# Kernel optimization log

Hardware: AMD Instinct MI355X
Metric: run time of the kernel (lower is better)

## Reference

```python
import math
import jax, jax.numpy as jnp
import numpy as np

# Dimensions (scalar irreps: o3.Irreps('8x0e').dim == 8, FullyConnectedTensorProduct
# between scalar irreps reduces to a learned bilinear map with a 3D weight tensor)
N = 50000       # nodes
C = 4           # channel dim ('c' in the einsum 'nci,neio->nceo')
DI = 8          # irreps_in.dim
DE = 8          # irreps_edge_attr.dim (must equal DI for the einsum to typecheck)
DO = 8          # irreps_out.dim (must equal DI for lin2 to consume the messages)
DA = 16         # irreps_node_attr.dim
E = 400000      # edges
F_EDGE = 32     # number_of_edge_features
H = 64          # radial_neurons
NUM_NEIGHBORS = 8


def setup_inputs() -> dict:
    key = jax.random.key(0)
    ks = jax.random.split(key, 12)
    inv = lambda f: 1.0 / np.sqrt(f)
    return {
        "node_input": jax.random.normal(ks[0], (N, C, DI), jnp.float32),
        "node_attr": jax.random.normal(ks[1], (N, DA), jnp.float32),
        "edge_features": jax.random.normal(ks[2], (E, F_EDGE), jnp.float32),
        # bilinear tensor-product weights (sc, lin1, lin2)
        "W_sc": jax.random.normal(ks[3], (DI, DA, DO), jnp.float32) * inv(DI * DA),
        "W_lin1": jax.random.normal(ks[4], (DI, DA, DI), jnp.float32) * inv(DI * DA),
        "W_lin2": jax.random.normal(ks[5], (DO, DA, DO), jnp.float32) * inv(DO * DA),
        # radial MLP: Linear(F_EDGE,H) -> SiLU -> Linear(H, DI*DE*DO)
        "fc_w1": jax.random.normal(ks[6], (F_EDGE, H), jnp.float32) * inv(F_EDGE),
        "fc_b1": jnp.zeros((H,), jnp.float32),
        "fc_w2": jax.random.normal(ks[7], (H, DI * DE * DO), jnp.float32) * inv(H),
        "fc_b2": jnp.zeros((DI * DE * DO,), jnp.float32),
        "edge_src": jax.random.randint(ks[8], (E,), 0, N, jnp.int32),
        "edge_dst": jax.random.randint(ks[9], (E,), 0, N, jnp.int32),
    }


def reference(node_input, node_attr, edge_features, W_sc, W_lin1, W_lin2,
              fc_w1, fc_b1, fc_w2, fc_b2, edge_src, edge_dst):
    n_nodes = node_input.shape[0]
    # self-connection and input linear (bilinear in node feature & node attr)
    s = jnp.einsum('nci,na,iao->nco', node_input, node_attr, W_sc)      # [N,C,DO]
    x = jnp.einsum('nci,na,iaj->ncj', node_input, node_attr, W_lin1)    # [N,C,DI]
    # radial MLP -> per-edge weight tensor [E, DI, DE, DO]
    h = jax.nn.silu(edge_features @ fc_w1 + fc_b1)
    ef = (h @ fc_w2 + fc_b2).reshape(-1, DI, DE, DO)
    # gather by source, per-edge contraction (einsum 'nci,neio->nceo'):
    # contract x's irrep dim with ef axis 2, keep ef axis 1 as output dim d
    msg = jnp.einsum('eci,edio->ecdo', x[edge_src], ef)                 # [E,C,DI,DO]
    # scatter-add to destination nodes
    agg = jax.ops.segment_sum(msg, edge_dst, num_segments=n_nodes)      # [N,C,DI,DO]
    agg = agg / jnp.sqrt(jnp.asarray(NUM_NEIGHBORS, agg.dtype))
    # output linear on the last (irreps_out) axis
    x2 = jnp.einsum('ncdo,na,oap->ncdp', agg, node_attr, W_lin2)        # [N,C,DI,DO]
    c_s = math.sin(math.pi / 8.0)
    # fully-connected scalar-irrep TP -> output_mask is all ones -> c_x scalar
    c_x = math.cos(math.pi / 8.0)
    return c_s * s[:, :, None, :] + c_x * x2
```

## Files before the change

kernel.cpp:

```cpp
#include <hip/hip_runtime.h>
#include <math.h>

#define CC 4
#define FE 32
#define HH 64
#define EBS 256
#define KEXT 544
#define ASTR 69

typedef __attribute__((ext_vector_type(8))) short bf16x8;
typedef __attribute__((ext_vector_type(4))) float f32x4;

__device__ inline unsigned short f2bf(float f) {
    unsigned u = __float_as_uint(f);
    u += 0x7fffu + ((u >> 16) & 1u);
    return (unsigned short)(u >> 16);
}
__device__ inline float bf2f(unsigned short b) {
    return __uint_as_float(((unsigned)b) << 16);
}

__global__ __launch_bounds__(256) void k_nodeprep(
    const float* __restrict__ node_input, const float* __restrict__ node_attr,
    const float* __restrict__ W_lin1, const float* __restrict__ W_sc,
    const float* __restrict__ W_lin2,
    float* __restrict__ xbuf, float* __restrict__ sbuf,
    float* __restrict__ w2n_ws, int N)
{
    const float c_s = 0.3826834323650898f;
    const float c_x_scaled = 0.9238795325112867f * 0.35355339059327373f;
    int node = blockIdx.x * 4 + (threadIdx.x >> 6);
    int lane = threadIdx.x & 63;
    if (node >= N) return;

    float attr_own = (lane < 16) ? node_attr[(size_t)node * 16 + lane] : 0.f;
    float ni_own   = (lane < 32) ? node_input[(size_t)node * 32 + lane] : 0.f;

    int iw = lane >> 3, jw = lane & 7;
    float wb1 = 0.f, wbs = 0.f, w2n = 0.f;
    #pragma unroll
    for (int a = 0; a < 16; ++a) {
        float fa = __shfl(attr_own, a);
        int idx = (iw * 16 + a) * 8 + jw;
        wb1 += fa * W_lin1[idx];
        wbs += fa * W_sc[idx];
        w2n += fa * W_lin2[idx];
    }
    w2n_ws[(size_t)node * 64 + lane] = c_x_scaled * w2n;

    int c_ = (lane >> 3) & 3, jo = lane & 7;
    float xo = 0.f, so = 0.f;
    #pragma unroll
    for (int i = 0; i < 8; ++i) {
        float niv = __shfl(ni_own, c_ * 8 + i);
        xo += niv * __shfl(wb1, i * 8 + jo);
        so += niv * __shfl(wbs, i * 8 + jo);
    }
    if (lane < 32) {
        xbuf[(size_t)node * 32 + lane] = xo;
        sbuf[(size_t)node * 32 + lane] = c_s * so;
    }
}

__global__ __launch_bounds__(256) void k_hist(
    const int* __restrict__ edge_dst, int* __restrict__ counts, int E)
{
    int e = blockIdx.x * 256 + threadIdx.x;
    if (e < E) atomicAdd(&counts[edge_dst[e]], 1);
}

__global__ __launch_bounds__(1024) void k_scanA(
    const int* __restrict__ counts, int* __restrict__ offsets,
    int* __restrict__ btot, int N)
{
    __shared__ int wsum[16];
    __shared__ int wpre[16];
    int tid = threadIdx.x, wid = tid >> 6, lane = tid & 63;
    int idx = blockIdx.x * 1024 + tid;
    int v = (idx < N) ? counts[idx] : 0;
    int x = v;
    #pragma unroll
    for (int s = 1; s < 64; s <<= 1) {
        int y = __shfl_up(x, s);
        if (lane >= s) x += y;
    }
    if (lane == 63) wsum[wid] = x;
    __syncthreads();
    if (wid == 0) {
        int wv = (lane < 16) ? wsum[lane] : 0;
        int wx = wv;
        #pragma unroll
        for (int s = 1; s < 16; s <<= 1) {
            int y = __shfl_up(wx, s);
            if (lane >= s) wx += y;
        }
        if (lane < 16) wpre[lane] = wx - wv;
    }
    __syncthreads();
    int excl = wpre[wid] + (x - v);
    if (idx < N) offsets[idx] = excl;
    if (tid == 1023) btot[blockIdx.x] = excl + v;
}

__global__ __launch_bounds__(1024) void k_scanB(int* __restrict__ btot, int nb)
{
    __shared__ int wsum[16];
    __shared__ int wpre[16];
    int tid = threadIdx.x, wid = tid >> 6, lane = tid & 63;
    int v = (tid < nb) ? btot[tid] : 0;
    int x = v;
    #pragma unroll
    for (int s = 1; s < 64; s <<= 1) {
        int y = __shfl_up(x, s);
        if (lane >= s) x += y;
    }
    if (lane == 63) wsum[wid] = x;
    __syncthreads();
    if (wid == 0) {
        int wv = (lane < 16) ? wsum[lane] : 0;
        int wx = wv;
        #pragma unroll
        for (int s = 1; s < 16; s <<= 1) {
            int y = __shfl_up(wx, s);
            if (lane >= s) wx += y;
        }
        if (lane < 16) wpre[lane] = wx - wv;
    }
    __syncthreads();
    if (tid < nb) btot[tid] = wpre[wid] + (x - v);
}

__global__ __launch_bounds__(256) void k_scanC(
    int* __restrict__ offsets, const int* __restrict__ btot,
    int* __restrict__ cursor, int N)
{
    int i = blockIdx.x * 256 + threadIdx.x;
    if (i < N) {
        int o = offsets[i] + btot[i >> 10];
        offsets[i] = o;
        cursor[i] = o;
    }
}

__global__ __launch_bounds__(256) void k_fill(
    const int* __restrict__ edge_dst, const int* __restrict__ edge_src,
    int* __restrict__ cursor, int* __restrict__ srcs, int* __restrict__ epos, int E)
{
    int e = blockIdx.x * 256 + threadIdx.x;
    if (e < E) {
        int pos = atomicAdd(&cursor[edge_dst[e]], 1);
        srcs[pos] = edge_src[e];
        epos[e] = pos;
    }
}

__global__ __launch_bounds__(256) void k_xgather(
    const int* __restrict__ srcs, const float* __restrict__ xin,
    float* __restrict__ xg, int E)
{
    int t = blockIdx.x * 256 + threadIdx.x;
    if (t >= E * 4) return;
    int pos = t >> 2, q = t & 3;
    int src = srcs[pos];
    const float4* xp = reinterpret_cast<const float4*>(xin + (size_t)src * 32 + q * 8);
    float4 a = xp[0], b = xp[1];
    float4* op = reinterpret_cast<float4*>(xg + (size_t)pos * 32 + q * 8);
    op[0] = a; op[1] = b;
}

__global__ __launch_bounds__(256) void k_prep_bfrag(
    const float* __restrict__ fc_w2, const float* __restrict__ fc_b2,
    unsigned short* __restrict__ Bfrag)
{
    int t = blockIdx.x * 256 + threadIdx.x;
    if (t >= KEXT * 64) return;
    int kappa = t >> 6, nu = t & 63;
    int d = nu >> 3, o = nu & 7;
    float val;
    if (kappa < 512)      val = fc_w2[(size_t)(kappa >> 3) * 512 + d * 64 + (kappa & 7) * 8 + o];
    else if (kappa < 520) val = fc_b2[d * 64 + (kappa & 7) * 8 + o];
    else                  val = 0.f;
    int kk = kappa >> 5;
    int lane = ((kappa >> 3) & 3) * 16 + (nu & 15);
    int ct = nu >> 4;
    int j = kappa & 7;
    Bfrag[(size_t)((kk * 4 + ct) * 64 + lane) * 8 + j] = f2bf(val);
}

__global__ __launch_bounds__(256) void k_prep_bfrag1(
    const float* __restrict__ fc_w1, unsigned short* __restrict__ Bfrag1)
{
    int t = blockIdx.x * 256 + threadIdx.x;
    if (t >= 4 * 64 * 8) return;
    int j = t & 7, l = (t >> 3) & 63, ct = t >> 9;
    int k = (l >> 4) * 8 + j;
    int n = ct * 16 + (l & 15);
    Bfrag1[t] = f2bf(fc_w1[(size_t)k * HH + n]);
}

__global__ __launch_bounds__(256) void k_hsilu(
    const float* __restrict__ edge_features,
    const unsigned short* __restrict__ Bfrag1, const float* __restrict__ fc_b1,
    const int* __restrict__ epos,
    unsigned short* __restrict__ H, int E)
{
    int wid = threadIdx.x >> 6, lane = threadIdx.x & 63;
    int e0 = (blockIdx.x * 4 + wid) * 16;
    if (e0 >= E) return;

    bf16x8 b[4];
    #pragma unroll
    for (int ct = 0; ct < 4; ++ct) {
        uint4 bv = reinterpret_cast<const uint4*>(Bfrag1)[ct * 64 + lane];
        b[ct] = *reinterpret_cast<bf16x8*>(&bv);
    }
    float bias[4];
    #pragma unroll
    for (int ct = 0; ct < 4; ++ct) bias[ct] = fc_b1[ct * 16 + (lane & 15)];

    int pr[4];
    #pragma unroll
    for (int v = 0; v < 4; ++v) {
        int r = e0 + (lane >> 4) * 4 + v;
        pr[v] = (r < E) ? epos[r] : -1;
    }

    int row = e0 + (lane & 15);
    if (row >= E) row = E - 1;
    const float4* ap = reinterpret_cast<const float4*>(
        edge_features + (size_t)row * FE + (lane >> 4) * 8);
    float4 a0 = ap[0], a1 = ap[1];
    unsigned au[4];
    au[0] = (unsigned)f2bf(a0.x) | ((unsigned)f2bf(a0.y) << 16);
    au[1] = (unsigned)f2bf(a0.z) | ((unsigned)f2bf(a0.w) << 16);
    au[2] = (unsigned)f2bf(a1.x) | ((unsigned)f2bf(a1.y) << 16);
    au[3] = (unsigned)f2bf(a1.z) | ((unsigned)f2bf(a1.w) << 16);
    bf16x8 a = *reinterpret_cast<bf16x8*>(au);

    f32x4 acc[4];
    #pragma unroll
    for (int ct = 0; ct < 4; ++ct) {
        acc[ct] = (f32x4){0.f, 0.f, 0.f, 0.f};
        acc[ct] = __builtin_amdgcn_mfma_f32_16x16x32_bf16(a, b[ct], acc[ct], 0, 0, 0);
    }

    #pragma unroll
    for (int ct = 0; ct < 4; ++ct) {
        #pragma unroll
        for (int v = 0; v < 4; ++v) {
            if (pr[v] >= 0) {
                float x = acc[ct][v] + bias[ct];
                float s = x / (1.f + __expf(-x));
                H[(size_t)pr[v] * HH + ct * 16 + (lane & 15)] = f2bf(s);
            }
        }
    }
}

__global__ __launch_bounds__(256) void k_zgemm(
    const unsigned short* __restrict__ H, const float* __restrict__ xg,
    const int* __restrict__ offsets, const int* __restrict__ counts,
    const unsigned short* __restrict__ Bfrag,
    float* __restrict__ out, int N)
{
    __shared__ uint4 alds[16 * ASTR];
    int wid = threadIdx.x >> 6, lane = threadIdx.x & 63;
    int node = blockIdx.x * 4 + wid;
    bool valid = (node < N);

    float z[CC][8];
    #pragma unroll
    for (int c = 0; c < CC; ++c)
        #pragma unroll
        for (int i = 0; i < 8; ++i) z[c][i] = 0.f;
    float xsown = 0.f;

    int off = 0, cnt = 0;
    if (valid) { off = offsets[node]; cnt = counts[node]; }
    #pragma unroll 2
    for (int j = 0; j < cnt; ++j) {
        size_t pos = (size_t)(off + j);
        float hk = bf2f(H[pos * HH + lane]);
        const float4* xp = reinterpret_cast<const float4*>(xg + pos * 32);
        float xs[32];
        #pragma unroll
        for (int q = 0; q < 8; ++q) {
            float4 v = xp[q];
            xs[q * 4 + 0] = v.x; xs[q * 4 + 1] = v.y;
            xs[q * 4 + 2] = v.z; xs[q * 4 + 3] = v.w;
        }
        #pragma unroll
        for (int c = 0; c < CC; ++c)
            #pragma unroll
            for (int i = 0; i < 8; ++i)
                z[c][i] += hk * xs[c * 8 + i];
        xsown += xg[pos * 32 + (lane & 31)];
    }

    #pragma unroll
    for (int c = 0; c < CC; ++c) {
        uint4 pk;
        pk.x = (unsigned)f2bf(z[c][0]) | ((unsigned)f2bf(z[c][1]) << 16);
        pk.y = (unsigned)f2bf(z[c][2]) | ((unsigned)f2bf(z[c][3]) << 16);
        pk.z = (unsigned)f2bf(z[c][4]) | ((unsigned)f2bf(z[c][5]) << 16);
        pk.w = (unsigned)f2bf(z[c][6]) | ((unsigned)f2bf(z[c][7]) << 16);
        alds[(wid * 4 + c) * ASTR + lane] = pk;
    }
    float xb[8];
    #pragma unroll
    for (int i = 0; i < 8; ++i) xb[i] = __shfl(xsown, (lane & 3) * 8 + i);
    int r4 = wid * 4;
    if (lane < 4) {
        uint4 pk;
        pk.x = (unsigned)f2bf(xb[0]) | ((unsigned)f2bf(xb[1]) << 16);
        pk.y = (unsigned)f2bf(xb[2]) | ((unsigned)f2bf(xb[3]) << 16);
        pk.z = (unsigned)f2bf(xb[4]) | ((unsigned)f2bf(xb[5]) << 16);
        pk.w = (unsigned)f2bf(xb[6]) | ((unsigned)f2bf(xb[7]) << 16);
        alds[(r4 + lane) * ASTR + 64] = pk;
    } else if (lane < 16) {
        int j = lane - 4;
        uint4 zz; zz.x = 0u; zz.y = 0u; zz.z = 0u; zz.w = 0u;
        alds[(r4 + (j & 3)) * ASTR + 65 + (j >> 2)] = zz;
    }

    bf16x8 bfr[17];
    #pragma unroll
    for (int kk = 0; kk < 16; ++kk) {
        uint4 bv = reinterpret_cast<const uint4*>(Bfrag)[(kk * 4 + wid) * 64 + lane];
        bfr[kk] = *reinterpret_cast<bf16x8*>(&bv);
    }
    {
        uint4 bv = reinterpret_cast<const uint4*>(Bfrag)[(64 + wid) * 64 + lane];
        bfr[16] = *reinterpret_cast<bf16x8*>(&bv);
    }

    __syncthreads();

    f32x4 acc = (f32x4){0.f, 0.f, 0.f, 0.f};
    #pragma unroll
    for (int kk = 0; kk < 16; ++kk) {
        uint4 av = alds[(lane & 15) * ASTR + kk * 4 + (lane >> 4)];
        bf16x8 a = *reinterpret_cast<bf16x8*>(&av);
        acc = __builtin_amdgcn_mfma_f32_16x16x32_bf16(a, bfr[kk], acc, 0, 0, 0);
    }
    {
        uint4 av = alds[(lane & 15) * ASTR + 64 + (lane >> 4)];
        bf16x8 a = *reinterpret_cast<bf16x8*>(&av);
        acc = __builtin_amdgcn_mfma_f32_16x16x32_bf16(a, bfr[16], acc, 0, 0, 0);
    }

    int rbase = blockIdx.x * 16;
    int M = N * 4;
    #pragma unroll
    for (int v = 0; v < 4; ++v) {
        int r = rbase + (lane >> 4) * 4 + v;
        if (r < M)
            out[(size_t)r * 64 + wid * 16 + (lane & 15)] = acc[v];
    }
}

__global__ __launch_bounds__(256) void k_node_out(
    const float* __restrict__ sbuf, const float* __restrict__ w2n_ws,
    float* __restrict__ out, int N)
{
    int node = blockIdx.x * 4 + (threadIdx.x >> 6);
    int lane = threadIdx.x & 63;
    if (node >= N) return;
    int d = lane >> 3, p = lane & 7;

    float w2 = w2n_ws[(size_t)node * 64 + lane];
    float s_own = sbuf[(size_t)node * 32 + (lane & 31)];

    float w2sh[8];
    #pragma unroll
    for (int o = 0; o < 8; ++o) w2sh[o] = __shfl(w2, o * 8 + p);

    float* rowp = out + (size_t)node * 256;
    #pragma unroll
    for (int c = 0; c < CC; ++c) {
        float a_own = rowp[c * 64 + lane];
        float res = 0.f;
        #pragma unroll
        for (int o = 0; o < 8; ++o)
            res += __shfl(a_own, d * 8 + o) * w2sh[o];
        float sval = __shfl(s_own, c * 8 + p);
        rowp[c * 64 + lane] = sval + res;
    }
}

__global__ __launch_bounds__(EBS) void k_edge_atomic(
    const float* __restrict__ edge_features,
    const float* __restrict__ fc_w1, const float* __restrict__ fc_b1,
    const float* __restrict__ fc_w2, const float* __restrict__ fc_b2,
    const int* __restrict__ edge_src, const int* __restrict__ edge_dst,
    const float* __restrict__ xin, float* __restrict__ agg, int E)
{
    __shared__ float hlds[HH * EBS];
    int e = blockIdx.x * EBS + threadIdx.x;
    if (e >= E) return;
    float h[HH];
    #pragma unroll
    for (int k = 0; k < HH; ++k) h[k] = fc_b1[k];
    const float4* efp = reinterpret_cast<const float4*>(edge_features + (size_t)e * FE);
    #pragma unroll
    for (int fq = 0; fq < FE / 4; ++fq) {
        float4 efv = efp[fq];
        float ev[4] = {efv.x, efv.y, efv.z, efv.w};
        #pragma unroll
        for (int fs = 0; fs < 4; ++fs) {
            float evv = ev[fs];
            const float4* w1p = reinterpret_cast<const float4*>(fc_w1 + (fq * 4 + fs) * HH);
            #pragma unroll
            for (int q = 0; q < HH / 4; ++q) {
                float4 w = w1p[q];
                h[q * 4 + 0] += evv * w.x;
                h[q * 4 + 1] += evv * w.y;
                h[q * 4 + 2] += evv * w.z;
                h[q * 4 + 3] += evv * w.w;
            }
        }
    }
    #pragma unroll
    for (int k = 0; k < HH; ++k) {
        float v = h[k];
        hlds[k * EBS + threadIdx.x] = v / (1.f + __expf(-v));
    }
    int src = edge_src[e], dst = edge_dst[e];
    float xs[32];
    const float4* xp = reinterpret_cast<const float4*>(xin + (size_t)src * 32);
    #pragma unroll
    for (int q = 0; q < 8; ++q) {
        float4 v = xp[q];
        xs[q * 4 + 0] = v.x; xs[q * 4 + 1] = v.y;
        xs[q * 4 + 2] = v.z; xs[q * 4 + 3] = v.w;
    }
    float* outp = agg + (size_t)dst * 256;
    #pragma unroll 1
    for (int d = 0; d < 8; ++d) {
        float t[64];
        const float4* b2p = reinterpret_cast<const float4*>(fc_b2 + d * 64);
        #pragma unroll
        for (int q = 0; q < 16; ++q) {
            float4 v = b2p[q];
            t[q * 4 + 0] = v.x; t[q * 4 + 1] = v.y;
            t[q * 4 + 2] = v.z; t[q * 4 + 3] = v.w;
        }
        for (int k = 0; k < HH; ++k) {
            float hv = hlds[k * EBS + threadIdx.x];
            const float4* wp = reinterpret_cast<const float4*>(fc_w2 + (size_t)k * 512 + d * 64);
            #pragma unroll
            for (int q = 0; q < 16; ++q) {
                float4 w = wp[q];
                t[q * 4 + 0] += hv * w.x;
                t[q * 4 + 1] += hv * w.y;
                t[q * 4 + 2] += hv * w.z;
                t[q * 4 + 3] += hv * w.w;
            }
        }
        #pragma unroll
        for (int c = 0; c < CC; ++c) {
            #pragma unroll
            for (int o = 0; o < 8; ++o) {
                float acc = 0.f;
                #pragma unroll
                for (int i = 0; i < 8; ++i) acc += xs[c * 8 + i] * t[i * 8 + o];
                atomicAdd(outp + c * 64 + d * 8 + o, acc);
            }
        }
    }
}

extern "C" void kernel_launch(void* const* d_in, const int* in_sizes, int n_in,
                              void* d_out, int out_size, void* d_ws, size_t ws_size,
                              hipStream_t stream)
{
    const float* node_input    = (const float*)d_in[0];
    const float* node_attr     = (const float*)d_in[1];
    const float* edge_features = (const float*)d_in[2];
    const float* W_sc          = (const float*)d_in[3];
    const float* W_lin1        = (const float*)d_in[4];
    const float* W_lin2        = (const float*)d_in[5];
    const float* fc_w1         = (const float*)d_in[6];
    const float* fc_b1         = (const float*)d_in[7];
    const float* fc_w2         = (const float*)d_in[8];
    const float* fc_b2         = (const float*)d_in[9];
    const int*   edge_src      = (const int*)d_in[10];
    const int*   edge_dst      = (const int*)d_in[11];

    const int N = in_sizes[1] / 16;
    const int E = in_sizes[10];
    const int nb = (N + 1023) / 1024;

    char* ws = (char*)d_ws;
    size_t off = 0;
    auto take = [&](size_t bytes) { char* p = ws + off; off += (bytes + 15) & ~(size_t)15; return p; };
    float* xbuf            = (float*)take((size_t)N * 32 * sizeof(float));
    float* sbuf            = (float*)take((size_t)N * 32 * sizeof(float));
    float* w2n_ws          = (float*)take((size_t)N * 64 * sizeof(float));
    int*   counts          = (int*)take((size_t)N * sizeof(int));
    int*   offsets         = (int*)take((size_t)N * sizeof(int));
    int*   cursor          = (int*)take((size_t)N * sizeof(int));
    int*   btot            = (int*)take((size_t)1024 * sizeof(int));
    int*   srcs            = (int*)take((size_t)E * sizeof(int));
    int*   epos            = (int*)take((size_t)E * sizeof(int));
    unsigned short* Bfrag  = (unsigned short*)take((size_t)17 * 4 * 64 * 8 * sizeof(unsigned short));
    unsigned short* Bfrag1 = (unsigned short*)take((size_t)4 * 64 * 8 * sizeof(unsigned short));
    unsigned short* Hbuf   = (unsigned short*)take((size_t)E * HH * sizeof(unsigned short));
    float* xg              = (float*)take((size_t)E * 32 * sizeof(float));
    bool fast = (off <= ws_size);

    float* out = (float*)d_out;

    k_nodeprep<<<(N + 3) / 4, 256, 0, stream>>>(
        node_input, node_attr, W_lin1, W_sc, W_lin2, xbuf, sbuf, w2n_ws, N);

    if (fast) {
        hipMemsetAsync(counts, 0, (size_t)N * sizeof(int), stream);
        k_hist<<<(E + 255) / 256, 256, 0, stream>>>(edge_dst, counts, E);
        k_scanA<<<nb, 1024, 0, stream>>>(counts, offsets, btot, N);
        k_scanB<<<1, 1024, 0, stream>>>(btot, nb);
        k_scanC<<<(N + 255) / 256, 256, 0, stream>>>(offsets, btot, cursor, N);
        k_fill<<<(E + 255) / 256, 256, 0, stream>>>(edge_dst, edge_src, cursor, srcs, epos, E);
        k_prep_bfrag1<<<(4 * 64 * 8 + 255) / 256, 256, 0, stream>>>(fc_w1, Bfrag1);
        k_prep_bfrag<<<(KEXT * 64 + 255) / 256, 256, 0, stream>>>(fc_w2, fc_b2, Bfrag);
        k_hsilu<<<(E + 63) / 64, 256, 0, stream>>>(edge_features, Bfrag1, fc_b1, epos, Hbuf, E);
        k_xgather<<<(E * 4 + 255) / 256, 256, 0, stream>>>(srcs, xbuf, xg, E);
        k_zgemm<<<(N + 3) / 4, 256, 0, stream>>>(
            Hbuf, xg, offsets, counts, Bfrag, out, N);
        k_node_out<<<(N + 3) / 4, 256, 0, stream>>>(sbuf, w2n_ws, out, N);
    } else {
        hipMemsetAsync(d_out, 0, (size_t)out_size * sizeof(float), stream);
        k_edge_atomic<<<(E + EBS - 1) / EBS, EBS, 0, stream>>>(
            edge_features, fc_w1, fc_b1, fc_w2, fc_b2, edge_src, edge_dst, xbuf, out, E);
        k_node_out<<<(N + 3) / 4, 256, 0, stream>>>(sbuf, w2n_ws, out, N);
    }
}
```

Before: 290.3 us.

## Sort nodes by in-degree to balance warps in the per-node edge GEMM

Adds a counting-sort pass (per-block degree histograms, a global scan, and a scatter) that builds a node permutation ordered by in-degree. k_zgemm then processes nodes in that order, so the four waves in a block walk edge loops of similar length, and it scatters results back to the original node rows. This aims to cut the idle time caused by degree imbalance within blocks. The cost is three extra small kernel launches and scattered output writes instead of contiguous ones.

New measurement: 296.2 us. 2.0% more time.

```diff
diff --git a/kernel.cpp b/kernel.cpp
--- a/kernel.cpp
+++ b/kernel.cpp
@@ -151,6 +151,75 @@
         int pos = atomicAdd(&cursor[edge_dst[e]], 1);
         srcs[pos] = edge_src[e];
         epos[e] = pos;
+    }
+}
+
+__global__ __launch_bounds__(1024) void k_dhistA(
+    const int* __restrict__ counts, int* __restrict__ bh, int N, int NB)
+{
+    __shared__ int h[64];
+    if (threadIdx.x < 64) h[threadIdx.x] = 0;
+    __syncthreads();
+    int i = blockIdx.x * 1024 + threadIdx.x;
+    if (i < N) {
+        int b = counts[i]; if (b > 63) b = 63;
+        atomicAdd(&h[b], 1);
+    }
+    __syncthreads();
+    if (threadIdx.x < 64) bh[threadIdx.x * NB + blockIdx.x] = h[threadIdx.x];
+}
+
+__global__ __launch_bounds__(1024) void k_dhistB(int* __restrict__ bh, int L)
+{
+    __shared__ int wsum[16];
+    __shared__ int wpre[16];
+    __shared__ int s_tot;
+    __shared__ int s_carry;
+    int tid = threadIdx.x, wid = tid >> 6, lane = tid & 63;
+    if (tid == 0) s_carry = 0;
+    __syncthreads();
+    for (int base = 0; base < L; base += 1024) {
+        int idx = base + tid;
+        int v = (idx < L) ? bh[idx] : 0;
+        int x = v;
+        #pragma unroll
+        for (int s = 1; s < 64; s <<= 1) {
+            int y = __shfl_up(x, s);
+            if (lane >= s) x += y;
+        }
+        if (lane == 63) wsum[wid] = x;
+        __syncthreads();
+        if (wid == 0) {
+            int wv = (lane < 16) ? wsum[lane] : 0;
+            int wx = wv;
+            #pragma unroll
+            for (int s = 1; s < 16; s <<= 1) {
+                int y = __shfl_up(wx, s);
+                if (lane >= s) wx += y;
+            }
+            if (lane < 16) wpre[lane] = wx - wv;
+            if (lane == 15) s_tot = wx;
+        }
+        __syncthreads();
+        if (idx < L) bh[idx] = s_carry + wpre[wid] + (x - v);
+        __syncthreads();
+        if (tid == 0) s_carry += s_tot;
+        __syncthreads();
+    }
+}
+
+__global__ __launch_bounds__(1024) void k_dscatter2(
+    const int* __restrict__ counts, const int* __restrict__ bh,
+    int* __restrict__ nodeperm, int N, int NB)
+{
+    __shared__ int cur[64];
+    if (threadIdx.x < 64) cur[threadIdx.x] = 0;
+    __syncthreads();
+    int i = blockIdx.x * 1024 + threadIdx.x;
+    if (i < N) {
+        int b = counts[i]; if (b > 63) b = 63;
+        int rank = atomicAdd(&cur[b], 1);
+        nodeperm[bh[b * NB + blockIdx.x] + rank] = i;
     }
 }
 
@@ -260,13 +329,15 @@
 __global__ __launch_bounds__(256) void k_zgemm(
     const unsigned short* __restrict__ H, const float* __restrict__ xg,
     const int* __restrict__ offsets, const int* __restrict__ counts,
+    const int* __restrict__ nodeperm,
     const unsigned short* __restrict__ Bfrag,
     float* __restrict__ out, int N)
 {
     __shared__ uint4 alds[16 * ASTR];
     int wid = threadIdx.x >> 6, lane = threadIdx.x & 63;
-    int node = blockIdx.x * 4 + wid;
-    bool valid = (node < N);
+    int nidx = blockIdx.x * 4 + wid;
+    bool valid = (nidx < N);
+    int node = valid ? nodeperm[nidx] : 0;
 
     float z[CC][8];
     #pragma unroll
@@ -349,13 +420,13 @@
         acc = __builtin_amdgcn_mfma_f32_16x16x32_bf16(a, bfr[16], acc, 0, 0, 0);
     }
 
-    int rbase = blockIdx.x * 16;
-    int M = N * 4;
-    #pragma unroll
-    for (int v = 0; v < 4; ++v) {
-        int r = rbase + (lane >> 4) * 4 + v;
-        if (r < M)
-            out[(size_t)r * 64 + wid * 16 + (lane & 15)] = acc[v];
+    int qslot = lane >> 4;
+    int nidx_q = blockIdx.x * 4 + qslot;
+    if (nidx_q < N) {
+        int rn = nodeperm[nidx_q];
+        #pragma unroll
+        for (int v = 0; v < 4; ++v)
+            out[(size_t)(rn * 4 + v) * 64 + wid * 16 + (lane & 15)] = acc[v];
     }
 }
 
@@ -501,6 +572,8 @@
     int*   offsets         = (int*)take((size_t)N * sizeof(int));
     int*   cursor          = (int*)take((size_t)N * sizeof(int));
     int*   btot            = (int*)take((size_t)1024 * sizeof(int));
+    int*   bh              = (int*)take((size_t)64 * nb * sizeof(int));
+    int*   nodeperm        = (int*)take((size_t)N * sizeof(int));
     int*   srcs            = (int*)take((size_t)E * sizeof(int));
     int*   epos            = (int*)take((size_t)E * sizeof(int));
     unsigned short* Bfrag  = (unsigned short*)take((size_t)17 * 4 * 64 * 8 * sizeof(unsigned short));
@@ -521,12 +594,15 @@
         k_scanB<<<1, 1024, 0, stream>>>(btot, nb);
         k_scanC<<<(N + 255) / 256, 256, 0, stream>>>(offsets, btot, cursor, N);
         k_fill<<<(E + 255) / 256, 256, 0, stream>>>(edge_dst, edge_src, cursor, srcs, epos, E);
+        k_dhistA<<<nb, 1024, 0, stream>>>(counts, bh, N, nb);
+        k_dhistB<<<1, 1024, 0, stream>>>(bh, 64 * nb);
+        k_dscatter2<<<nb, 1024, 0, stream>>>(counts, bh, nodeperm, N, nb);
         k_prep_bfrag1<<<(4 * 64 * 8 + 255) / 256, 256, 0, stream>>>(fc_w1, Bfrag1);
         k_prep_bfrag<<<(KEXT * 64 + 255) / 256, 256, 0, stream>>>(fc_w2, fc_b2, Bfrag);
         k_hsilu<<<(E + 63) / 64, 256, 0, stream>>>(edge_features, Bfrag1, fc_b1, epos, Hbuf, E);
         k_xgather<<<(E * 4 + 255) / 256, 256, 0, stream>>>(srcs, xbuf, xg, E);
         k_zgemm<<<(N + 3) / 4, 256, 0, stream>>>(
-            Hbuf, xg, offsets, counts, Bfrag, out, N);
+            Hbuf, xg, offsets, counts, nodeperm, Bfrag, out, N);
         k_node_out<<<(N + 3) / 4, 256, 0, stream>>>(sbuf, w2n_ws, out, N);
     } else {
         hipMemsetAsync(d_out, 0, (size_t)out_size * sizeof(float), stream);
```

## Drop materialized x-gather; read source rows and H indirectly in zgemm

Applied to the files above, without the earlier changes.

Removes the k_xgather kernel and the E×32 float gathered buffer. k_fill now writes (edge id, src) pairs in CSR order, and k_hsilu writes H in original edge order without the epos scatter. k_zgemm loads the pairs 64 at a time per wave, broadcasts them with shuffles, and reads H rows and x rows indirectly. This cuts a large write/read round trip (about 51 MB) and one kernel launch. In exchange, H reads in zgemm are no longer contiguous and x rows are gathered randomly, where they may hit in cache.

Measured after the change: 273.2 us, median of 2. -5.9%, faster.

```diff
diff --git a/kernel.cpp b/kernel.cpp
--- a/kernel.cpp
+++ b/kernel.cpp
@@ -144,28 +144,14 @@
 
 __global__ __launch_bounds__(256) void k_fill(
     const int* __restrict__ edge_dst, const int* __restrict__ edge_src,
-    int* __restrict__ cursor, int* __restrict__ srcs, int* __restrict__ epos, int E)
+    int* __restrict__ cursor, int2* __restrict__ esrc, int E)
 {
     int e = blockIdx.x * 256 + threadIdx.x;
     if (e < E) {
         int pos = atomicAdd(&cursor[edge_dst[e]], 1);
-        srcs[pos] = edge_src[e];
-        epos[e] = pos;
-    }
-}
-
-__global__ __launch_bounds__(256) void k_xgather(
-    const int* __restrict__ srcs, const float* __restrict__ xin,
-    float* __restrict__ xg, int E)
-{
-    int t = blockIdx.x * 256 + threadIdx.x;
-    if (t >= E * 4) return;
-    int pos = t >> 2, q = t & 3;
-    int src = srcs[pos];
-    const float4* xp = reinterpret_cast<const float4*>(xin + (size_t)src * 32 + q * 8);
-    float4 a = xp[0], b = xp[1];
-    float4* op = reinterpret_cast<float4*>(xg + (size_t)pos * 32 + q * 8);
-    op[0] = a; op[1] = b;
+        int2 v; v.x = e; v.y = edge_src[e];
+        esrc[pos] = v;
+    }
 }
 
 __global__ __launch_bounds__(256) void k_prep_bfrag(
@@ -201,7 +187,6 @@
 __global__ __launch_bounds__(256) void k_hsilu(
     const float* __restrict__ edge_features,
     const unsigned short* __restrict__ Bfrag1, const float* __restrict__ fc_b1,
-    const int* __restrict__ epos,
     unsigned short* __restrict__ H, int E)
 {
     int wid = threadIdx.x >> 6, lane = threadIdx.x & 63;
@@ -217,13 +202,6 @@
     float bias[4];
     #pragma unroll
     for (int ct = 0; ct < 4; ++ct) bias[ct] = fc_b1[ct * 16 + (lane & 15)];
-
-    int pr[4];
-    #pragma unroll
-    for (int v = 0; v < 4; ++v) {
-        int r = e0 + (lane >> 4) * 4 + v;
-        pr[v] = (r < E) ? epos[r] : -1;
-    }
 
     int row = e0 + (lane & 15);
     if (row >= E) row = E - 1;
@@ -248,19 +226,20 @@
     for (int ct = 0; ct < 4; ++ct) {
         #pragma unroll
         for (int v = 0; v < 4; ++v) {
-            if (pr[v] >= 0) {
+            int r = e0 + (lane >> 4) * 4 + v;
+            if (r < E) {
                 float x = acc[ct][v] + bias[ct];
                 float s = x / (1.f + __expf(-x));
-                H[(size_t)pr[v] * HH + ct * 16 + (lane & 15)] = f2bf(s);
+                H[(size_t)r * HH + ct * 16 + (lane & 15)] = f2bf(s);
             }
         }
     }
 }
 
 __global__ __launch_bounds__(256) void k_zgemm(
-    const unsigned short* __restrict__ H, const float* __restrict__ xg,
+    const unsigned short* __restrict__ H, const int2* __restrict__ esrc,
     const int* __restrict__ offsets, const int* __restrict__ counts,
-    const unsigned short* __restrict__ Bfrag,
+    const float* __restrict__ xin, const unsigned short* __restrict__ Bfrag,
     float* __restrict__ out, int N)
 {
     __shared__ uint4 alds[16 * ASTR];
@@ -277,24 +256,29 @@
 
     int off = 0, cnt = 0;
     if (valid) { off = offsets[node]; cnt = counts[node]; }
-    #pragma unroll 2
-    for (int j = 0; j < cnt; ++j) {
-        size_t pos = (size_t)(off + j);
-        float hk = bf2f(H[pos * HH + lane]);
-        const float4* xp = reinterpret_cast<const float4*>(xg + pos * 32);
-        float xs[32];
-        #pragma unroll
-        for (int q = 0; q < 8; ++q) {
-            float4 v = xp[q];
-            xs[q * 4 + 0] = v.x; xs[q * 4 + 1] = v.y;
-            xs[q * 4 + 2] = v.z; xs[q * 4 + 3] = v.w;
-        }
-        #pragma unroll
-        for (int c = 0; c < CC; ++c)
+    for (int base = 0; base < cnt; base += 64) {
+        int m = (cnt - base < 64) ? (cnt - base) : 64;
+        int2 ej = (lane < m) ? esrc[off + base + lane] : make_int2(0, 0);
+        #pragma unroll 2
+        for (int j = 0; j < m; ++j) {
+            int e   = __shfl(ej.x, j);
+            int src = __shfl(ej.y, j);
+            float hk = bf2f(H[(size_t)e * HH + lane]);
+            const float4* xp = reinterpret_cast<const float4*>(xin + (size_t)src * 32);
+            float xs[32];
             #pragma unroll
-            for (int i = 0; i < 8; ++i)
-                z[c][i] += hk * xs[c * 8 + i];
-        xsown += xg[pos * 32 + (lane & 31)];
+            for (int q = 0; q < 8; ++q) {
+                float4 v = xp[q];
+                xs[q * 4 + 0] = v.x; xs[q * 4 + 1] = v.y;
+                xs[q * 4 + 2] = v.z; xs[q * 4 + 3] = v.w;
+            }
+            #pragma unroll
+            for (int c = 0; c < CC; ++c)
+                #pragma unroll
+                for (int i = 0; i < 8; ++i)
+                    z[c][i] += hk * xs[c * 8 + i];
+            xsown += xin[(size_t)src * 32 + (lane & 31)];
+        }
     }
 
     #pragma unroll
@@ -501,12 +485,10 @@
     int*   offsets         = (int*)take((size_t)N * sizeof(int));
     int*   cursor          = (int*)take((size_t)N * sizeof(int));
     int*   btot            = (int*)take((size_t)1024 * sizeof(int));
-    int*   srcs            = (int*)take((size_t)E * sizeof(int));
-    int*   epos            = (int*)take((size_t)E * sizeof(int));
+    int2*  esrc            = (int2*)take((size_t)E * sizeof(int2));
     unsigned short* Bfrag  = (unsigned short*)take((size_t)17 * 4 * 64 * 8 * sizeof(unsigned short));
     unsigned short* Bfrag1 = (unsigned short*)take((size_t)4 * 64 * 8 * sizeof(unsigned short));
     unsigned short* Hbuf   = (unsigned short*)take((size_t)E * HH * sizeof(unsigned short));
-    float* xg              = (float*)take((size_t)E * 32 * sizeof(float));
     bool fast = (off <= ws_size);
 
     float* out = (float*)d_out;
@@ -520,13 +502,12 @@
         k_scanA<<<nb, 1024, 0, stream>>>(counts, offsets, btot, N);
         k_scanB<<<1, 1024, 0, stream>>>(btot, nb);
         k_scanC<<<(N + 255) / 256, 256, 0, stream>>>(offsets, btot, cursor, N);
-        k_fill<<<(E + 255) / 256, 256, 0, stream>>>(edge_dst, edge_src, cursor, srcs, epos, E);
+        k_fill<<<(E + 255) / 256, 256, 0, stream>>>(edge_dst, edge_src, cursor, esrc, E);
         k_prep_bfrag1<<<(4 * 64 * 8 + 255) / 256, 256, 0, stream>>>(fc_w1, Bfrag1);
         k_prep_bfrag<<<(KEXT * 64 + 255) / 256, 256, 0, stream>>>(fc_w2, fc_b2, Bfrag);
-        k_hsilu<<<(E + 63) / 64, 256, 0, stream>>>(edge_features, Bfrag1, fc_b1, epos, Hbuf, E);
-        k_xgather<<<(E * 4 + 255) / 256, 256, 0, stream>>>(srcs, xbuf, xg, E);
+        k_hsilu<<<(E + 63) / 64, 256, 0, stream>>>(edge_features, Bfrag1, fc_b1, Hbuf, E);
         k_zgemm<<<(N + 3) / 4, 256, 0, stream>>>(
-            Hbuf, xg, offsets, counts, Bfrag, out, N);
+            Hbuf, esrc, offsets, counts, xbuf, Bfrag, out, N);
         k_node_out<<<(N + 3) / 4, 256, 0, stream>>>(sbuf, w2n_ws, out, N);
     } else {
         hipMemsetAsync(d_out, 0, (size_t)out_size * sizeof(float), stream);
```
